# Performance work log

Measured on AMD Instinct MI355X. Metric: run time of the kernel, lower is better.

Reference implementation:

```python
import jax, jax.numpy as jnp
import numpy as np

EPS = 1e-06
ALPHA = 0.5
SIGMA = 50.0
INF = 1e12  # 'infinity' for empty cells; INF + L^2 stays representable in fp32


def _dt_last(f):
    """Exact 1D squared Euclidean distance transform along the last axis:
    out[..., i] = min_j f[..., j] + (i - j)^2  (min-plus with parabola kernel).
    Scanned over output index i to avoid materializing an [..., L, L] tensor."""
    L = f.shape[-1]
    idx = jnp.arange(L)

    def step(carry, i):
        row = jnp.min(f + ((i - idx) ** 2).astype(f.dtype), axis=-1)
        return carry, row

    _, out = jax.lax.scan(step, None, idx)  # [L, ...batch]
    return jnp.moveaxis(out, 0, -1)


def _edt(mask):
    """Euclidean distance from every pixel to the nearest True pixel, per sample.
    mask: [B, H, W] bool. Equivalent to scipy.ndimage.distance_transform_edt(~mask)."""
    f = jnp.where(mask, jnp.float32(0.0), jnp.float32(INF))
    f = jnp.swapaxes(_dt_last(jnp.swapaxes(f, 1, 2)), 1, 2)  # pass along H
    f = _dt_last(f)                                          # pass along W
    return jnp.sqrt(f)


def _weight_map(targets):
    mask = targets > 0
    dist = _edt(mask)
    w = 1.0 - jnp.exp(-dist / SIGMA)
    has_fg = jnp.any(mask, axis=(1, 2))  # torch code leaves weight 0 for empty masks
    return jnp.where(has_fg[:, None, None], w, jnp.float32(0.0))


def setup_inputs() -> dict:
    key = jax.random.key(0)
    k1, k2 = jax.random.split(key)
    B, H, W = 16, 512, 512
    logits = jax.random.normal(k1, (B, H, W), dtype=jnp.float32)
    targets = (jax.random.uniform(k2, (B, H, W)) < 0.01).astype(jnp.float32)
    return {"logits": logits, "targets": targets}


def reference(logits, targets):
    probs = jax.nn.sigmoid(logits)
    inter = jnp.sum(probs * targets)
    union = jnp.sum(probs) + jnp.sum(targets) - inter
    soft_iou_loss = 1.0 - (inter + EPS) / (union + EPS)
    weight = _weight_map(targets)
    distance_penalty = jnp.mean(weight * probs * (1.0 - targets))
    return soft_iou_loss + ALPHA * distance_penalty
```

## Files before the change

kernel.cpp:

```cpp
#include <hip/hip_runtime.h>
#include <math.h>

#define BB 16
#define HH 512
#define WW 512
#define NPIX (BB*HH*WW)
#define NWORDS 16
#define HB 256
#define HWORDS 8
#define NBLK 1024

__device__ inline unsigned int even16(unsigned int x) {
  x &= 0x55555555u;
  x = (x | (x >> 1)) & 0x33333333u;
  x = (x | (x >> 2)) & 0x0F0F0F0Fu;
  x = (x | (x >> 4)) & 0x00FF00FFu;
  x = (x | (x >> 8)) & 0x0000FFFFu;
  return x;
}

__global__ __launch_bounds__(256) void build_kernel(
    const float* __restrict__ tg, unsigned int* __restrict__ mask,
    unsigned int* __restrict__ hmask, short* __restrict__ un_h,
    short* __restrict__ dn_h) {
  __shared__ unsigned int smask[NWORDS][32];
  __shared__ unsigned int hsm[HWORDS][16];
  int wt = blockIdx.x & 15;
  int b  = blockIdx.x >> 4;
  int c2 = threadIdx.x & 15;
  int k  = threadIdx.x >> 4;
  int w  = (wt << 5) + (c2 << 1);
  const float* p = tg + ((size_t)(b * HH + (k << 5))) * WW + w;
  unsigned int w0 = 0, w1 = 0;
  #pragma unroll
  for (int r = 0; r < 32; ++r) {
    float2 v = *(const float2*)&p[(size_t)r * WW];
    w0 |= (v.x > 0.f ? 1u : 0u) << r;
    w1 |= (v.y > 0.f ? 1u : 0u) << r;
  }
  smask[k][(c2 << 1)] = w0;
  smask[k][(c2 << 1) + 1] = w1;
  *(uint2*)&mask[(b * NWORDS + k) * WW + w] = make_uint2(w0, w1);
  __syncthreads();
  int t = threadIdx.x;
  if (t < 128) {
    int kp  = t >> 4;
    int bcl = t & 15;
    unsigned int wa = smask[2 * kp][2 * bcl] | smask[2 * kp][2 * bcl + 1];
    unsigned int wb = smask[2 * kp + 1][2 * bcl] | smask[2 * kp + 1][2 * bcl + 1];
    unsigned int hword = even16(wa | (wa >> 1)) | (even16(wb | (wb >> 1)) << 16);
    hsm[kp][bcl] = hword;
    hmask[(b * HWORDS + kp) * HB + (wt << 4) + bcl] = hword;
  }
  __syncthreads();
  if (t < 16) {
    int bc = (wt << 4) + t;
    int cur = 16000;
    un_h[(b * 9 + 8) * HB + bc] = (short)cur;
    #pragma unroll
    for (int kp = HWORDS - 1; kp >= 0; --kp) {
      unsigned int m = hsm[kp][t];
      if (m) cur = (kp << 5) + (int)__builtin_ctz(m);
      un_h[(b * 9 + kp) * HB + bc] = (short)cur;
    }
  } else if (t >= 64 && t < 80) {
    int tt = t - 64;
    int bc = (wt << 4) + tt;
    int cur = -16000;
    dn_h[(b * 9 + 0) * HB + bc] = (short)cur;
    #pragma unroll
    for (int kp = 0; kp < HWORDS; ++kp) {
      unsigned int m = hsm[kp][tt];
      if (m) cur = (kp << 5) + 31 - (int)__builtin_clz(m);
      dn_h[(b * 9 + kp + 1) * HB + bc] = (short)cur;
    }
  }
}

__global__ __launch_bounds__(256) void edt_loss_kernel(
    const float* __restrict__ logits, const unsigned int* __restrict__ mask,
    const unsigned int* __restrict__ hmask, const short* __restrict__ un_h,
    const short* __restrict__ dn_h, float* __restrict__ partials) {
  __shared__ __align__(16) float sraw[256 + HB + 256];
  __shared__ __align__(8) float sw[HB];
  __shared__ float wsum[4][4];
  float* sA = sraw + 256;

  int g = blockIdx.x;
  int b = g >> 6, Rbase = (g & 63) << 2;
  int tid = threadIdx.x;

  sraw[tid] = 3e12f;
  sraw[256 + HB + tid] = 3e12f;

  int ir = tid >> 7;
  int wc = (tid & 127) << 2;
  size_t lbase = ((size_t)(b * HH + (Rbase << 1) + ir)) * WW + wc;
  float4 x4_0 = *(const float4*)&logits[lbase];
  float4 x4_1 = *(const float4*)&logits[lbase + 2 * WW];
  float4 x4_2 = *(const float4*)&logits[lbase + 4 * WW];
  float4 x4_3 = *(const float4*)&logits[lbase + 6 * WW];
  uint4 mw_0 = *(const uint4*)&mask[(b * NWORDS + (((Rbase << 1) + ir) >> 5)) * WW + wc];
  uint4 mw_1 = *(const uint4*)&mask[(b * NWORDS + (((Rbase << 1) + 2 + ir) >> 5)) * WW + wc];
  uint4 mw_2 = *(const uint4*)&mask[(b * NWORDS + (((Rbase << 1) + 4 + ir) >> 5)) * WW + wc];
  uint4 mw_3 = *(const uint4*)&mask[(b * NWORDS + (((Rbase << 1) + 6 + ir) >> 5)) * WW + wc];

  float acc_p = 0.f, acc_t = 0.f, acc_pt = 0.f, acc_pen = 0.f;

#define PX(XC, WC, MC)                                      \
  { float x = (XC);                                         \
    float tt = (float)(((MC) >> bit) & 1u);                 \
    float e = __expf(-x);                                   \
    float pp = __builtin_amdgcn_rcpf(1.f + e);              \
    acc_p += pp; acc_t += tt; acc_pt += pp * tt;            \
    acc_pen += (WC) * pp * (1.f - tt); }

#define ROW_BODY(J, X4, MW)                                                   \
  {                                                                           \
    int R = Rbase + (J);                                                      \
    int k0 = R >> 5, pos = R & 31;                                            \
    unsigned int pmask_lo = (1u << pos) - 1u;                                 \
    unsigned int pmask_le = pmask_lo | (1u << pos);                           \
    unsigned int m0 = hmask[(b * HWORDS + k0) * HB + tid];                    \
    int un_next = un_h[(b * 9 + k0 + 1) * HB + tid];                          \
    int dn_prev = dn_h[(b * 9 + k0) * HB + tid];                              \
    unsigned int upm  = m0 & ~pmask_lo;                                       \
    unsigned int lowm = m0 & pmask_le;                                        \
    int up  = upm  ? ((k0 << 5) + (int)__builtin_ctz(upm))       : un_next;   \
    int dnv = lowm ? ((k0 << 5) + 31 - (int)__builtin_clz(lowm)) : dn_prev;   \
    int bv = min(up - R, R - dnv);                                            \
    float dv = (bv > 255) ? 1e12f : (float)(bv * bv);                         \
    sA[tid] = dv;                                                             \
    __syncthreads();                                                          \
    float best = dv;                                                          \
    for (int o0 = 1; o0 < HB; o0 += 8) {                                      \
      if (__all((float)(o0 * o0) >= best)) break;                             \
      _Pragma("unroll")                                                       \
      for (int u = 0; u < 8; ++u) {                                           \
        int o = o0 + u;                                                       \
        best = fminf(best, fminf(sA[tid - o], sA[tid + o]) + (float)(o * o)); \
      }                                                                       \
    }                                                                         \
    sw[tid] = (best > 1e9f)                                                   \
                  ? 0.f                                                       \
                  : (1.f - __expf(-__builtin_amdgcn_sqrtf(best) * 0.04f));    \
    __syncthreads();                                                          \
    int i = ((R) << 1) + ir;                                                  \
    int bit = i & 31;                                                         \
    float2 wv = *(const float2*)&sw[wc >> 1];                                 \
    PX(X4.x, wv.x, MW.x)                                                      \
    PX(X4.y, wv.x, MW.y)                                                      \
    PX(X4.z, wv.y, MW.z)                                                      \
    PX(X4.w, wv.y, MW.w)                                                      \
    __syncthreads();                                                          \
  }

  ROW_BODY(0, x4_0, mw_0)
  ROW_BODY(1, x4_1, mw_1)
  ROW_BODY(2, x4_2, mw_2)
  ROW_BODY(3, x4_3, mw_3)
#undef ROW_BODY
#undef PX

  #pragma unroll
  for (int off = 32; off; off >>= 1) {
    acc_p  += __shfl_down(acc_p,  off);
    acc_t  += __shfl_down(acc_t,  off);
    acc_pt += __shfl_down(acc_pt, off);
    acc_pen += __shfl_down(acc_pen, off);
  }
  int wave = tid >> 6, lane = tid & 63;
  if (lane == 0) {
    wsum[wave][0] = acc_p; wsum[wave][1] = acc_t;
    wsum[wave][2] = acc_pt; wsum[wave][3] = acc_pen;
  }
  __syncthreads();
  if (tid == 0) {
    float r0 = 0.f, r1 = 0.f, r2 = 0.f, r3 = 0.f;
    #pragma unroll
    for (int wv2 = 0; wv2 < 4; ++wv2) {
      r0 += wsum[wv2][0]; r1 += wsum[wv2][1];
      r2 += wsum[wv2][2]; r3 += wsum[wv2][3];
    }
    partials[0 * NBLK + g] = r0;
    partials[1 * NBLK + g] = r1;
    partials[2 * NBLK + g] = r2;
    partials[3 * NBLK + g] = r3;
  }
}

__global__ __launch_bounds__(256) void finalize_kernel(
    const float* __restrict__ partials, float* __restrict__ out) {
  __shared__ float wsum[4][4];
  int tid = threadIdx.x;
  float a0 = 0.f, a1 = 0.f, a2 = 0.f, a3 = 0.f;
  for (int k = tid; k < NBLK; k += 256) {
    a0 += partials[0 * NBLK + k];
    a1 += partials[1 * NBLK + k];
    a2 += partials[2 * NBLK + k];
    a3 += partials[3 * NBLK + k];
  }
  #pragma unroll
  for (int off = 32; off; off >>= 1) {
    a0 += __shfl_down(a0, off);
    a1 += __shfl_down(a1, off);
    a2 += __shfl_down(a2, off);
    a3 += __shfl_down(a3, off);
  }
  int wave = tid >> 6, lane = tid & 63;
  if (lane == 0) {
    wsum[wave][0] = a0; wsum[wave][1] = a1;
    wsum[wave][2] = a2; wsum[wave][3] = a3;
  }
  __syncthreads();
  if (tid == 0) {
    float sp = 0.f, st = 0.f, inter = 0.f, pen = 0.f;
    #pragma unroll
    for (int wv = 0; wv < 4; ++wv) {
      sp += wsum[wv][0]; st += wsum[wv][1];
      inter += wsum[wv][2]; pen += wsum[wv][3];
    }
    float uni = sp + st - inter;
    float iou_loss = 1.f - (inter + 1e-6f) / (uni + 1e-6f);
    float penalty = pen / (float)NPIX;
    out[0] = iou_loss + 0.5f * penalty;
  }
}

extern "C" void kernel_launch(void* const* d_in, const int* in_sizes, int n_in,
                              void* d_out, int out_size, void* d_ws, size_t ws_size,
                              hipStream_t stream) {
  const float* logits = (const float*)d_in[0];
  const float* tg     = (const float*)d_in[1];
  char* base = (char*)d_ws;
  unsigned int* mask  = (unsigned int*)base;
  unsigned int* hmask = (unsigned int*)(base + 524288);
  short* un_h = (short*)(base + 655360);
  short* dn_h = (short*)(base + 729088);
  float* partials = (float*)(base + 802816);
  float* out = (float*)d_out;

  hipLaunchKernelGGL(build_kernel, dim3(256), dim3(256), 0, stream,
                     tg, mask, hmask, un_h, dn_h);
  hipLaunchKernelGGL(edt_loss_kernel, dim3(NBLK), dim3(256), 0, stream,
                     logits, mask, hmask, un_h, dn_h, partials);
  hipLaunchKernelGGL(finalize_kernel, dim3(1), dim3(256), 0, stream,
                     partials, out);
}
```

Before: 21.83 us.

## Assign one half-res row per wave with four columns per lane in EDT pass

Restructures the loss kernel so each wavefront owns one half-resolution row and each lane handles four adjacent columns. The horizontal min-plus scan now uses vectorised float2 LDS reads shared across the four columns, and only one block-wide barrier is needed instead of three per row. The price is more registers per thread and an early-exit vote taken on the max over four columns, which can run more iterations. Logits and mask loads now come after the scan instead of being prefetched at kernel start.

New measurement: 19.44 us (median of 2 runs). -11.0%, faster.

```diff
diff --git a/kernel.cpp b/kernel.cpp
--- a/kernel.cpp
+++ b/kernel.cpp
@@ -81,85 +81,99 @@
     const float* __restrict__ logits, const unsigned int* __restrict__ mask,
     const unsigned int* __restrict__ hmask, const short* __restrict__ un_h,
     const short* __restrict__ dn_h, float* __restrict__ partials) {
-  __shared__ __align__(16) float sraw[256 + HB + 256];
-  __shared__ __align__(8) float sw[HB];
+  __shared__ __align__(16) float srow[4][768];
   __shared__ float wsum[4][4];
-  float* sA = sraw + 256;
 
   int g = blockIdx.x;
   int b = g >> 6, Rbase = (g & 63) << 2;
   int tid = threadIdx.x;
-
-  sraw[tid] = 3e12f;
-  sraw[256 + HB + tid] = 3e12f;
-
-  int ir = tid >> 7;
-  int wc = (tid & 127) << 2;
-  size_t lbase = ((size_t)(b * HH + (Rbase << 1) + ir)) * WW + wc;
-  float4 x4_0 = *(const float4*)&logits[lbase];
-  float4 x4_1 = *(const float4*)&logits[lbase + 2 * WW];
-  float4 x4_2 = *(const float4*)&logits[lbase + 4 * WW];
-  float4 x4_3 = *(const float4*)&logits[lbase + 6 * WW];
-  uint4 mw_0 = *(const uint4*)&mask[(b * NWORDS + (((Rbase << 1) + ir) >> 5)) * WW + wc];
-  uint4 mw_1 = *(const uint4*)&mask[(b * NWORDS + (((Rbase << 1) + 2 + ir) >> 5)) * WW + wc];
-  uint4 mw_2 = *(const uint4*)&mask[(b * NWORDS + (((Rbase << 1) + 4 + ir) >> 5)) * WW + wc];
-  uint4 mw_3 = *(const uint4*)&mask[(b * NWORDS + (((Rbase << 1) + 6 + ir) >> 5)) * WW + wc];
+  int wv = tid >> 6, lane = tid & 63;
+  int R = Rbase + wv;
+  int c0 = lane << 2;
+  float* sA = &srow[wv][256];
+
+  *(float4*)&srow[wv][lane << 2] = make_float4(3e12f, 3e12f, 3e12f, 3e12f);
+  *(float4*)&srow[wv][512 + (lane << 2)] = make_float4(3e12f, 3e12f, 3e12f, 3e12f);
+
+  int k0 = R >> 5, pos = R & 31;
+  unsigned int pmask_lo = (1u << pos) - 1u;
+  unsigned int pmask_le = pmask_lo | (1u << pos);
+  int kb = k0 << 5;
+  uint4 hm = *(const uint4*)&hmask[(b * HWORDS + k0) * HB + c0];
+  short4 un4 = *(const short4*)&un_h[(b * 9 + k0 + 1) * HB + c0];
+  short4 dn4 = *(const short4*)&dn_h[(b * 9 + k0) * HB + c0];
+
+  float dv0, dv1, dv2, dv3;
+#define VERT(MC, UNC, DNC, DVOUT)                                         \
+  { unsigned int upm  = (MC) & ~pmask_lo;                                 \
+    unsigned int lowm = (MC) & pmask_le;                                  \
+    int up  = upm  ? (kb + (int)__builtin_ctz(upm))        : (int)(UNC);  \
+    int dnv = lowm ? (kb + 31 - (int)__builtin_clz(lowm))  : (int)(DNC);  \
+    int bv = min(up - R, R - dnv);                                        \
+    DVOUT = (bv > 255) ? 1e12f : (float)(bv * bv); }
+  VERT(hm.x, un4.x, dn4.x, dv0)
+  VERT(hm.y, un4.y, dn4.y, dv1)
+  VERT(hm.z, un4.z, dn4.z, dv2)
+  VERT(hm.w, un4.w, dn4.w, dv3)
+#undef VERT
+  *(float4*)&sA[c0] = make_float4(dv0, dv1, dv2, dv3);
+  __syncthreads();
+
+  float b0 = dv0, b1 = dv1, b2 = dv2, b3 = dv3;
+  for (int o0 = 1; o0 < HB; o0 += 8) {
+    float bmax = fmaxf(fmaxf(b0, b1), fmaxf(b2, b3));
+    if (__all((float)(o0 * o0) >= bmax)) break;
+    const float2* Lp = (const float2*)&sA[c0 - o0 - 7];
+    const float2* Rp = (const float2*)&sA[c0 + o0 - 1];
+    float2 L0 = Lp[0], L1 = Lp[1], L2 = Lp[2], L3 = Lp[3], L4 = Lp[4], L5 = Lp[5];
+    float2 R0 = Rp[0], R1 = Rp[1], R2 = Rp[2], R3 = Rp[3], R4 = Rp[4], R5 = Rp[5];
+#define STEP(U, A0, B0, A1, B1, A2, B2, A3, B3)             \
+    { float oo = (float)((o0 + (U)) * (o0 + (U)));          \
+      b0 = fminf(b0, fminf((A0), (B0)) + oo);               \
+      b1 = fminf(b1, fminf((A1), (B1)) + oo);               \
+      b2 = fminf(b2, fminf((A2), (B2)) + oo);               \
+      b3 = fminf(b3, fminf((A3), (B3)) + oo); }
+    STEP(0, L3.y, R0.y, L4.x, R1.x, L4.y, R1.y, L5.x, R2.x)
+    STEP(1, L3.x, R1.x, L3.y, R1.y, L4.x, R2.x, L4.y, R2.y)
+    STEP(2, L2.y, R1.y, L3.x, R2.x, L3.y, R2.y, L4.x, R3.x)
+    STEP(3, L2.x, R2.x, L2.y, R2.y, L3.x, R3.x, L3.y, R3.y)
+    STEP(4, L1.y, R2.y, L2.x, R3.x, L2.y, R3.y, L3.x, R4.x)
+    STEP(5, L1.x, R3.x, L1.y, R3.y, L2.x, R4.x, L2.y, R4.y)
+    STEP(6, L0.y, R3.y, L1.x, R4.x, L1.y, R4.y, L2.x, R5.x)
+    STEP(7, L0.x, R4.x, L0.y, R4.y, L1.x, R5.x, L1.y, R5.y)
+#undef STEP
+  }
+
+#define WGT(BC) (((BC) > 1e9f) ? 0.f \
+                 : (1.f - __expf(-__builtin_amdgcn_sqrtf(BC) * 0.04f)))
+  float wg0 = WGT(b0), wg1 = WGT(b1), wg2 = WGT(b2), wg3 = WGT(b3);
+#undef WGT
 
   float acc_p = 0.f, acc_t = 0.f, acc_pt = 0.f, acc_pen = 0.f;
-
-#define PX(XC, WC, MC)                                      \
+  int wcl = lane << 3;
+#define PX(XC, WC, MC, BIT)                                 \
   { float x = (XC);                                         \
-    float tt = (float)(((MC) >> bit) & 1u);                 \
+    float tt = (float)(((MC) >> (BIT)) & 1u);               \
     float e = __expf(-x);                                   \
     float pp = __builtin_amdgcn_rcpf(1.f + e);              \
     acc_p += pp; acc_t += tt; acc_pt += pp * tt;            \
     acc_pen += (WC) * pp * (1.f - tt); }
-
-#define ROW_BODY(J, X4, MW)                                                   \
-  {                                                                           \
-    int R = Rbase + (J);                                                      \
-    int k0 = R >> 5, pos = R & 31;                                            \
-    unsigned int pmask_lo = (1u << pos) - 1u;                                 \
-    unsigned int pmask_le = pmask_lo | (1u << pos);                           \
-    unsigned int m0 = hmask[(b * HWORDS + k0) * HB + tid];                    \
-    int un_next = un_h[(b * 9 + k0 + 1) * HB + tid];                          \
-    int dn_prev = dn_h[(b * 9 + k0) * HB + tid];                              \
-    unsigned int upm  = m0 & ~pmask_lo;                                       \
-    unsigned int lowm = m0 & pmask_le;                                        \
-    int up  = upm  ? ((k0 << 5) + (int)__builtin_ctz(upm))       : un_next;   \
-    int dnv = lowm ? ((k0 << 5) + 31 - (int)__builtin_clz(lowm)) : dn_prev;   \
-    int bv = min(up - R, R - dnv);                                            \
-    float dv = (bv > 255) ? 1e12f : (float)(bv * bv);                         \
-    sA[tid] = dv;                                                             \
-    __syncthreads();                                                          \
-    float best = dv;                                                          \
-    for (int o0 = 1; o0 < HB; o0 += 8) {                                      \
-      if (__all((float)(o0 * o0) >= best)) break;                             \
-      _Pragma("unroll")                                                       \
-      for (int u = 0; u < 8; ++u) {                                           \
-        int o = o0 + u;                                                       \
-        best = fminf(best, fminf(sA[tid - o], sA[tid + o]) + (float)(o * o)); \
-      }                                                                       \
-    }                                                                         \
-    sw[tid] = (best > 1e9f)                                                   \
-                  ? 0.f                                                       \
-                  : (1.f - __expf(-__builtin_amdgcn_sqrtf(best) * 0.04f));    \
-    __syncthreads();                                                          \
-    int i = ((R) << 1) + ir;                                                  \
-    int bit = i & 31;                                                         \
-    float2 wv = *(const float2*)&sw[wc >> 1];                                 \
-    PX(X4.x, wv.x, MW.x)                                                      \
-    PX(X4.y, wv.x, MW.y)                                                      \
-    PX(X4.z, wv.y, MW.z)                                                      \
-    PX(X4.w, wv.y, MW.w)                                                      \
-    __syncthreads();                                                          \
-  }
-
-  ROW_BODY(0, x4_0, mw_0)
-  ROW_BODY(1, x4_1, mw_1)
-  ROW_BODY(2, x4_2, mw_2)
-  ROW_BODY(3, x4_3, mw_3)
-#undef ROW_BODY
+#define ROW_LOSS(RR)                                                        \
+  { int i = (R << 1) + (RR);                                                \
+    int bit = i & 31;                                                       \
+    size_t lb = ((size_t)(b * HH + i)) * WW + wcl;                          \
+    const unsigned int* mrow = &mask[(b * NWORDS + (i >> 5)) * WW + wcl];   \
+    float4 xA = *(const float4*)&logits[lb];                                \
+    float4 xB = *(const float4*)&logits[lb + 4];                            \
+    uint4 mA = *(const uint4*)&mrow[0];                                     \
+    uint4 mB = *(const uint4*)&mrow[4];                                     \
+    PX(xA.x, wg0, mA.x, bit) PX(xA.y, wg0, mA.y, bit)                       \
+    PX(xA.z, wg1, mA.z, bit) PX(xA.w, wg1, mA.w, bit)                       \
+    PX(xB.x, wg2, mB.x, bit) PX(xB.y, wg2, mB.y, bit)                       \
+    PX(xB.z, wg3, mB.z, bit) PX(xB.w, wg3, mB.w, bit) }
+  ROW_LOSS(0)
+  ROW_LOSS(1)
+#undef ROW_LOSS
 #undef PX
 
   #pragma unroll
@@ -169,18 +183,17 @@
     acc_pt += __shfl_down(acc_pt, off);
     acc_pen += __shfl_down(acc_pen, off);
   }
-  int wave = tid >> 6, lane = tid & 63;
   if (lane == 0) {
-    wsum[wave][0] = acc_p; wsum[wave][1] = acc_t;
-    wsum[wave][2] = acc_pt; wsum[wave][3] = acc_pen;
+    wsum[wv][0] = acc_p; wsum[wv][1] = acc_t;
+    wsum[wv][2] = acc_pt; wsum[wv][3] = acc_pen;
   }
   __syncthreads();
   if (tid == 0) {
     float r0 = 0.f, r1 = 0.f, r2 = 0.f, r3 = 0.f;
     #pragma unroll
-    for (int wv2 = 0; wv2 < 4; ++wv2) {
-      r0 += wsum[wv2][0]; r1 += wsum[wv2][1];
-      r2 += wsum[wv2][2]; r3 += wsum[wv2][3];
+    for (int q = 0; q < 4; ++q) {
+      r0 += wsum[q][0]; r1 += wsum[q][1];
+      r2 += wsum[q][2]; r3 += wsum[q][3];
     }
     partials[0 * NBLK + g] = r0;
     partials[1 * NBLK + g] = r1;
```
